# Optimization experiments

Hardware: AMD Instinct MI355X
Metric: run time of the kernel (lower is better)

The kernel has to match this reference:

```python
import jax, jax.numpy as jnp
import numpy as np
from jax import lax

# dims
B, T_MEL, N_MEL, L_TXT, D_TXT = 8, 400, 80, 128, 512
E, HID, EMB, N_SPK = 256, 256, 128, 100
H = HID // 2  # per-direction LSTM hidden


def setup_inputs() -> dict:
    key = jax.random.key(0)
    ks = jax.random.split(key, 16)
    def n(k, shape, s=0.02):
        return jax.random.normal(k, shape, jnp.float32) * s
    return {
        "x": n(ks[0], (B, N_MEL, T_MEL), 1.0),
        "input_lengths": jax.random.randint(ks[1], (B,), T_MEL // 2, T_MEL + 1).astype(jnp.int32),
        "text": n(ks[2], (B, L_TXT, D_TXT), 1.0),
        "text_lengths": jax.random.randint(ks[3], (B,), L_TXT // 2, L_TXT + 1).astype(jnp.int32),
        "Wx": n(ks[4], (E, N_MEL)), "bx": jnp.zeros((E,), jnp.float32),
        "Wq": n(ks[5], (E, D_TXT)), "bq": jnp.zeros((E,), jnp.float32),
        "Wout": n(ks[6], (E, E)), "bout": jnp.zeros((E,), jnp.float32),
        "v": jax.random.normal(ks[7], (E, 1), jnp.float32) * 0.1,
        "lstm_wih": n(ks[8], (2, 2, 4 * H, HID)),
        "lstm_whh": n(ks[9], (2, 2, 4 * H, H)),
        "lstm_bih": jnp.zeros((2, 2, 4 * H), jnp.float32),
        "lstm_bhh": jnp.zeros((2, 2, 4 * H), jnp.float32),
        "p1_w": n(ks[10], (EMB, HID)), "p1_b": jnp.zeros((EMB,), jnp.float32),
        "p2_w": n(ks[11], (N_SPK, EMB)), "p2_b": jnp.zeros((N_SPK,), jnp.float32),
    }


def _run_lstm(x, Wih, Whh, bih, bhh):
    # x: [B, L, in] -> outputs [B, L, H]; PyTorch gate order i,f,g,o
    h0 = jnp.zeros((x.shape[0], Whh.shape[1]), x.dtype)
    c0 = jnp.zeros_like(h0)
    def step(carry, xt):
        h, c = carry
        g = xt @ Wih.T + h @ Whh.T + (bih + bhh)
        i, f, gg, o = jnp.split(g, 4, axis=-1)
        c = jax.nn.sigmoid(f) * c + jax.nn.sigmoid(i) * jnp.tanh(gg)
        h = jax.nn.sigmoid(o) * jnp.tanh(c)
        return (h, c), h
    _, hs = lax.scan(step, (h0, c0), x.swapaxes(0, 1))  # scan over time
    return hs.swapaxes(0, 1)


def _reverse_by_length(x, lengths):
    # reverse the first lengths[b] steps of each sequence (pack_padded semantics)
    L = x.shape[1]
    idx = jnp.clip(lengths[:, None] - 1 - jnp.arange(L)[None, :], 0, L - 1)
    return jnp.take_along_axis(x, idx[:, :, None], axis=1)


def reference(x, input_lengths, text, text_lengths, Wx, bx, Wq, bq, Wout, bout, v,
              lstm_wih, lstm_whh, lstm_bih, lstm_bhh, p1_w, p1_b, p2_w, p2_b):
    # ---- vectorized VanillaAttention over all text tokens ----
    mels = x.swapaxes(1, 2)                       # [B, T, M]
    x1 = mels @ Wx.T + bx                         # [B, T, E]   linear_x
    q1 = text @ Wq.T + bq                         # [B, L, E]   linear_q
    # v^T @ out_linear(tanh(.)) == tanh(.) @ (Wout^T v) + v . bout
    w = Wout.T @ v[:, 0]                          # [E]
    c = bout @ v[:, 0]                            # scalar
    s = jnp.tanh(x1[:, None, :, :] + q1[:, :, None, :])   # [B, L, T, E]
    scores = jnp.einsum('blte,e->blt', s, w) + c           # [B, L, T]
    mel_mask = jnp.arange(T_MEL)[None, :] < input_lengths[:, None]   # [B, T]
    scores = jnp.where(mel_mask[:, None, :], scores, -jnp.inf)
    scores = jax.nn.softmax(scores, axis=-1)
    contexts = jnp.einsum('blt,bte->ble', scores, x1)       # [B, L, E]
    h = q1 + contexts                                       # LSTM input

    # ---- 2-layer bidirectional LSTM (packed semantics via per-length reversal) ----
    for layer in range(2):
        fwd = _run_lstm(h, lstm_wih[layer, 0], lstm_whh[layer, 0], lstm_bih[layer, 0], lstm_bhh[layer, 0])
        rev = _reverse_by_length(h, text_lengths)
        bwd = _run_lstm(rev, lstm_wih[layer, 1], lstm_whh[layer, 1], lstm_bih[layer, 1], lstm_bhh[layer, 1])
        bwd = _reverse_by_length(bwd, text_lengths)
        h = jnp.concatenate([fwd, bwd], axis=-1)            # [B, L, HID]

    # ---- masked mean pool (pad_packed zeros the padding before the sum) ----
    txt_mask = (jnp.arange(L_TXT)[None, :] < text_lengths[:, None]).astype(h.dtype)
    pooled = (h * txt_mask[:, :, None]).sum(axis=1) / text_lengths[:, None].astype(h.dtype)

    out = jnp.tanh(pooled @ p1_w.T + p1_b)
    embeddings = out / jnp.linalg.norm(out, axis=1, keepdims=True)
    logits = out @ p2_w.T + p2_b
    return logits, embeddings, scores
```

## Files before the change

### kernel.cpp

```cpp
#include <hip/hip_runtime.h>
#include <hip/hip_bf16.h>
#include <math.h>

#define B 8
#define T_MEL 400
#define N_MEL 80
#define L_TXT 128
#define D_TXT 512
#define E 256
#define HID 256
#define EMB 128
#define N_SPK 100
#define HH 128

#define OFF_W      0
#define OFF_C      256
#define OFF_WXT    272
#define OFF_WQT    (OFF_WXT + N_MEL*E)
#define OFF_WIHT   (OFF_WQT + D_TXT*E)
#define OFF_BSUM   (OFF_WIHT + 2*2*256*512)
#define OFF_X1     (OFF_BSUM + 2048)
#define OFF_Q1     (OFF_X1 + B*T_MEL*E)
#define OFF_G      OFF_X1
#define OFF_H0     (OFF_Q1 + B*L_TXT*E)
#define OFF_O1     (OFF_H0 + B*L_TXT*E)
#define OFF_HS0    OFF_H0
#define OFF_POOL   OFF_O1
#define OFF_WG     (OFF_O1 + 4096)

typedef _Float16 half2v __attribute__((ext_vector_type(2)));

__device__ __forceinline__ float fast_sigmoid(float x){ return 1.f/(1.f+__expf(-x)); }
__device__ __forceinline__ float fast_tanh(float x){ float e=__expf(2.f*x); return 1.f - 2.f/(e+1.f); }

__device__ __forceinline__ float fdot2(uint a, uint b, float c){
  half2v ha = __builtin_bit_cast(half2v, a);
  half2v hb = __builtin_bit_cast(half2v, b);
#if __has_builtin(__builtin_amdgcn_fdot2)
  return __builtin_amdgcn_fdot2(ha, hb, c, false);
#else
  float r;
  asm("v_dot2_f32_f16 %0, %1, %2, %3" : "=v"(r) : "v"(a), "v"(b), "v"(c));
  return r;
#endif
}
__device__ __forceinline__ uint packh2(float a, float b){
  union { _Float16 h[2]; uint u; } x;
  x.h[0] = (_Float16)a; x.h[1] = (_Float16)b; return x.u;
}

__global__ __launch_bounds__(256) void k_prep(const float* __restrict__ Wout, const float* __restrict__ bout,
                       const float* __restrict__ v,    const float* __restrict__ Wx,
                       const float* __restrict__ Wq,   const float* __restrict__ wih,
                       const float* __restrict__ bih,  const float* __restrict__ bhh,
                       const float* __restrict__ whh,  float* __restrict__ ws){
  int blk = blockIdx.x, tid = threadIdx.x;
  if (blk == 0){
    float acc = 0.f;
    for (int j=0;j<E;j++) acc += Wout[j*E + tid] * v[j];
    ws[OFF_W + tid] = acc;
    if (tid==0){ float c=0.f; for(int j=0;j<E;j++) c += bout[j]*v[j]; ws[OFF_C]=c; }
  } else if (blk <= N_MEL){
    int m = blk-1;
    ws[OFF_WXT + m*E + tid] = Wx[tid*N_MEL + m];
  } else if (blk <= N_MEL + D_TXT){
    int k = blk-1-N_MEL;
    ws[OFF_WQT + k*E + tid] = Wq[tid*D_TXT + k];
  } else if (blk <= N_MEL + D_TXT + 512){
    int idx = blk-1-N_MEL-D_TXT;
    int ld = idx >> 7, k2 = idx & 127;
    uint* wout = (uint*)(ws + OFF_WIHT) + (size_t)idx*512;
    for (int g = tid; g < 512; g += 256){
      float a = wih[((size_t)(ld*512+g))*256 + 2*k2];
      float b = wih[((size_t)(ld*512+g))*256 + 2*k2 + 1];
      wout[g] = packh2(a, b);
    }
  } else if (blk == 1105){
    for (int i = tid; i < 2048; i += 256)
      ws[OFF_BSUM + i] = bih[i] + bhh[i];
  } else {
    int bp = blk - 1106;
    int ld = bp >> 2, w = bp & 3;
    uint* wg = (uint*)(ws + OFF_WG) + ((size_t)ld*4 + w)*8192;
    for (int ii = 0; ii < 32; ii++){
      int i = ii*256 + tid;
      int r  = i >> 11;
      int jj = (i >> 8) & 7;
      int l  = (i >> 2) & 63;
      int k  = i & 3;
      int u  = w*32 + (l >> 1);
      int hf = l & 1;
      const float* src = whh + ((size_t)(ld*512 + r*128 + u))*HH + 64*hf + jj*8 + 2*k;
      wg[i] = packh2(src[0], src[1]);
    }
  }
}

__global__ __launch_bounds__(256) void k_xq(const float* __restrict__ x,    const float* __restrict__ bx,
                                            const float* __restrict__ text, const float* __restrict__ bq,
                                            float* __restrict__ ws){
  __shared__ float sbuf[2048];
  int blk = blockIdx.x, tid = threadIdx.x;
  if (blk < 800){
    int b = blk/100; int t0 = (blk%100)*4;
    float (*sx)[4] = (float(*)[4])sbuf;
    for (int i = tid; i < N_MEL*4; i += 256){
      int m = i>>2, ii = i&3;
      sx[m][ii] = x[(b*N_MEL+m)*T_MEL + t0 + ii];
    }
    __syncthreads();
    float bxe = bx[tid];
    float a0=bxe,a1=bxe,a2=bxe,a3=bxe;
    const float* wxt = ws + OFF_WXT;
    #pragma unroll 4
    for (int m=0;m<N_MEL;m++){
      float w = wxt[m*E + tid];
      a0 += sx[m][0]*w; a1 += sx[m][1]*w; a2 += sx[m][2]*w; a3 += sx[m][3]*w;
    }
    float* x1 = ws + OFF_X1 + (b*T_MEL + t0)*E + tid;
    x1[0]=a0; x1[E]=a1; x1[2*E]=a2; x1[3*E]=a3;
  } else {
    int bb = blk - 800;
    int b = bb/32; int l0 = (bb%32)*4;
    float (*st)[D_TXT] = (float(*)[D_TXT])sbuf;
    for (int i = tid; i < 4*D_TXT; i += 256){
      int li = i / D_TXT, k = i % D_TXT;
      st[li][k] = text[(b*L_TXT + l0 + li)*D_TXT + k];
    }
    __syncthreads();
    float bqe = bq[tid];
    float a0=bqe,a1=bqe,a2=bqe,a3=bqe;
    const float* wqt = ws + OFF_WQT;
    #pragma unroll 2
    for (int k=0;k<D_TXT;k++){
      float w = wqt[k*E + tid];
      a0 += st[0][k]*w; a1 += st[1][k]*w; a2 += st[2][k]*w; a3 += st[3][k]*w;
    }
    float* q1 = ws + OFF_Q1 + (b*L_TXT + l0)*E + tid;
    q1[0]=a0; q1[E]=a1; q1[2*E]=a2; q1[3*E]=a3;
  }
}

__global__ __launch_bounds__(256) void k_score(const int* __restrict__ mel_len,
                                               float* __restrict__ ws,
                                               float* __restrict__ d_out){
  int blk = blockIdx.x; int b = blk >> 7; int l = blk & 127;
  int tid = threadIdx.x; int lane = tid & 63; int wv = tid >> 6;
  __shared__ __align__(16) float sl[T_MEL];
  __shared__ float red[8];
  const float* x1 = ws + OFF_X1 + b*T_MEL*E;
  const float* q1 = ws + OFF_Q1 + (b*L_TXT+l)*E;
  int g = lane >> 4, i = lane & 15;
  float qv[16], wvv[16];
  {
    const float4* q4 = (const float4*)(q1 + i*16);
    const float4* w4 = (const float4*)(ws + OFF_W + i*16);
    #pragma unroll
    for (int j=0;j<4;j++){
      float4 a = q4[j]; qv[4*j]=a.x; qv[4*j+1]=a.y; qv[4*j+2]=a.z; qv[4*j+3]=a.w;
      float4 c = w4[j]; wvv[4*j]=c.x; wvv[4*j+1]=c.y; wvv[4*j+2]=c.z; wvv[4*j+3]=c.w;
    }
  }
  float cc = ws[OFF_C];
  int len = mel_len[b];
  #pragma unroll 2
  for (int iter=0; iter<25; iter++){
    int t = iter*16 + wv*4 + g;
    const float4* xr = (const float4*)(x1 + t*E + i*16);
    float s = 0.f;
    #pragma unroll
    for (int j=0;j<4;j++){
      float4 xv = xr[j];
      s += wvv[4*j+0]*fast_tanh(xv.x + qv[4*j+0]);
      s += wvv[4*j+1]*fast_tanh(xv.y + qv[4*j+1]);
      s += wvv[4*j+2]*fast_tanh(xv.z + qv[4*j+2]);
      s += wvv[4*j+3]*fast_tanh(xv.w + qv[4*j+3]);
    }
    s += __shfl_xor(s,1); s += __shfl_xor(s,2);
    s += __shfl_xor(s,4); s += __shfl_xor(s,8);
    if (i==0) sl[t] = s + cc;
  }
  __syncthreads();
  float mx = -3.0e38f;
  for (int t = tid; t < T_MEL; t += 256) if (t < len) mx = fmaxf(mx, sl[t]);
  #pragma unroll
  for (int off=32; off>=1; off>>=1) mx = fmaxf(mx, __shfl_xor(mx, off));
  if (lane==0) red[wv] = mx;
  __syncthreads();
  mx = fmaxf(fmaxf(red[0],red[1]),fmaxf(red[2],red[3]));
  float se = 0.f;
  for (int t = tid; t < T_MEL; t += 256){
    float p = (t < len) ? __expf(sl[t]-mx) : 0.f;
    sl[t] = p; se += p;
  }
  #pragma unroll
  for (int off=32; off>=1; off>>=1) se += __shfl_xor(se, off);
  if (lane==0) red[4+wv] = se;
  __syncthreads();
  float rsum = 1.f/(red[4]+red[5]+red[6]+red[7]);
  float* sc_out = d_out + 1824 + (b*L_TXT + l)*T_MEL;
  for (int t = tid; t < T_MEL; t += 256){
    float p = sl[t]*rsum;
    sl[t] = p; sc_out[t] = p;
  }
  __syncthreads();
  float a = 0.f;
  int e = tid;
  for (int t = 0; t < T_MEL; t += 4){
    float4 p4 = *(const float4*)&sl[t];
    a += p4.x*x1[(t  )*E+e] + p4.y*x1[(t+1)*E+e]
       + p4.z*x1[(t+2)*E+e] + p4.w*x1[(t+3)*E+e];
  }
  ws[OFF_H0 + (b*L_TXT+l)*E + e] = q1[e] + a;
}

__global__ __launch_bounds__(512) void k_gates(const float* __restrict__ in,
                                               const float* __restrict__ hs,
                                               const int* __restrict__ txt_len,
                                               float* __restrict__ gates, int layer,
                                               float* __restrict__ ws){
  int idx = blockIdx.x; int tt = idx & 15; int dir = (idx>>4)&1; int b = idx>>5;
  int tid = threadIdx.x;
  __shared__ __align__(16) uint sih[8][128];
  int len = txt_len[b];
  for (int i = tid; i < 8*128; i += 512){
    int r = i >> 7, k2 = i & 127;
    int t = tt*8 + r;
    int row = dir ? max(0, len-1-t) : t;
    float va, vb;
    if (layer == 0){
      const float2 p = *(const float2*)&in[((size_t)(b*L_TXT + row))*HID + 2*k2];
      va = p.x; vb = p.y;
    } else {
      int k = 2*k2; int d = k >> 7, u = k & 127;
      int sidx = (d==0) ? row : (row < len ? len-1-row : 0);
      const float* hr = hs + (((size_t)(d*8+b)*128) + u)*128 + sidx;
      va = hr[0]; vb = hr[128];
    }
    sih[r][k2] = packh2(va, vb);
  }
  __syncthreads();
  int ld = layer*2 + dir;
  int g = tid;
  float bsum = ws[OFF_BSUM + ld*512 + g];
  float acc[8];
  #pragma unroll
  for (int r=0;r<8;r++) acc[r] = bsum;
  const uint* wt2 = (const uint*)(ws + OFF_WIHT) + (size_t)ld*128*512 + g;
  for (int k4=0; k4<128; k4+=4){
    uint w0 = wt2[(k4  )*512];
    uint w1 = wt2[(k4+1)*512];
    uint w2 = wt2[(k4+2)*512];
    uint w3 = wt2[(k4+3)*512];
    #pragma unroll
    for (int r=0;r<8;r++){
      uint4 s4 = *(const uint4*)&sih[r][k4];
      acc[r] = fdot2(s4.x, w0, acc[r]);
      acc[r] = fdot2(s4.y, w1, acc[r]);
      acc[r] = fdot2(s4.z, w2, acc[r]);
      acc[r] = fdot2(s4.w, w3, acc[r]);
    }
  }
  float* go = gates + (((size_t)(dir*L_TXT + tt*8)*8) + b)*512 + g;
  #pragma unroll
  for (int r=0;r<8;r++) go[(size_t)r*8*512] = acc[r];
}

__global__ __launch_bounds__(256) void k_scan(const float* __restrict__ Gp,
                                              const float* __restrict__ whh_all,
                                              const uint* __restrict__ wg,
                                              const int* __restrict__ txt_len,
                                              float* __restrict__ hseq,
                                              float* __restrict__ pooled, int layer){
  int dir = blockIdx.x & 1; int b = blockIdx.x >> 1;
  int tid = threadIdx.x;
  int l = tid & 63, w = tid >> 6;
  int u  = tid >> 1;
  int hf = tid & 1;

  __shared__ uint wlds[16384];
  __shared__ uint h2buf[2][64];

  const float* wbase = whh_all + (size_t)(layer*2+dir)*512*HH;
  #pragma unroll
  for (int r=0;r<2;r++){
    const float* wr = wbase + (size_t)(r*128+u)*HH + 64*hf;
    #pragma unroll
    for (int jj=0;jj<8;jj++){
      uint4 vv;
      vv.x = packh2(wr[jj*8+0], wr[jj*8+1]);
      vv.y = packh2(wr[jj*8+2], wr[jj*8+3]);
      vv.z = packh2(wr[jj*8+4], wr[jj*8+5]);
      vv.w = packh2(wr[jj*8+6], wr[jj*8+7]);
      *(uint4*)(wlds + w*4096 + (r*8+jj)*256 + l*4) = vv;
    }
  }
  if (tid < 128) ((uint*)h2buf)[tid] = 0;
  int len = txt_len[b];
  bool pool = (layer == 1);

  const float* gb = Gp + ((size_t)(dir*L_TXT)*8 + b)*512 + u;
  float g0 = gb[0], g1 = gb[128], g2 = gb[256], g3 = gb[384];
  float c_reg = 0.f, psum = 0.f;
  float hm1=0.f, hm2=0.f, hm3=0.f;
  __syncthreads();

  const uint4* wp  = (const uint4*)(wlds + w*4096 + l*4);
  const uint*  wgp = wg + (((size_t)(layer*2+dir))*4 + w)*8192 + l*4;
  float* hout = hseq + (((size_t)(dir*8+b)*128) + u)*128;

  for (int s=0; s<L_TXT; s++){
    const float* gn = gb + (size_t)(s+1 < L_TXT ? s+1 : s)*4096;
    float n0 = gn[0], n1 = gn[128], n2 = gn[256], n3 = gn[384];
    const uint4* hp = (const uint4*)(h2buf[s&1] + hf*32);
    float a0 = hf ? 0.f : g0;
    float a1 = hf ? 0.f : g1;
    float a2 = hf ? 0.f : g2;
    float a3 = hf ? 0.f : g3;
    #pragma unroll
    for (int jj=0;jj<8;jj++){
      uint4 hv = hp[jj];
      uint4 w0 = wp[(jj   )*64];
      uint4 w1 = wp[( 8+jj)*64];
      uint4 w2 = *(const uint4*)(wgp + (16+jj)*256);
      uint4 w3 = *(const uint4*)(wgp + (24+jj)*256);
      a0 = fdot2(w0.x,hv.x,a0); a0 = fdot2(w0.y,hv.y,a0);
      a0 = fdot2(w0.z,hv.z,a0); a0 = fdot2(w0.w,hv.w,a0);
      a1 = fdot2(w1.x,hv.x,a1); a1 = fdot2(w1.y,hv.y,a1);
      a1 = fdot2(w1.z,hv.z,a1); a1 = fdot2(w1.w,hv.w,a1);
      a2 = fdot2(w2.x,hv.x,a2); a2 = fdot2(w2.y,hv.y,a2);
      a2 = fdot2(w2.z,hv.z,a2); a2 = fdot2(w2.w,hv.w,a2);
      a3 = fdot2(w3.x,hv.x,a3); a3 = fdot2(w3.y,hv.y,a3);
      a3 = fdot2(w3.z,hv.z,a3); a3 = fdot2(w3.w,hv.w,a3);
    }
    a0 += __shfl_xor(a0, 1);
    a1 += __shfl_xor(a1, 1);
    a2 += __shfl_xor(a2, 1);
    a3 += __shfl_xor(a3, 1);
    float i_ = fast_sigmoid(a0);
    float f_ = fast_sigmoid(a1);
    float g_ = fast_tanh   (a2);
    float o_ = fast_sigmoid(a3);
    c_reg = f_*c_reg + i_*g_;
    float h = o_*fast_tanh(c_reg);
    float hn = __shfl_xor(h, 2);
    if (hf==0 && !(u&1)) h2buf[(s+1)&1][u>>1] = packh2(h, hn);
    if (pool){
      if (s < len) psum += h;
    } else {
      if (hf==0 && (s&3)==3)
        *(float4*)&hout[s-3] = make_float4(hm3, hm2, hm1, h);
      hm3 = hm2; hm2 = hm1; hm1 = h;
    }
    g0 = n0; g1 = n1; g2 = n2; g3 = n3;
    __syncthreads();
  }
  if (pool && hf==0) pooled[((size_t)(dir*8+b))*128 + u] = psum;
}

__global__ __launch_bounds__(256) void k_final(const float* __restrict__ pooled,
                                               const int* __restrict__ txt_len,
                                               const float* __restrict__ p1w,
                                               const float* __restrict__ p1b,
                                               const float* __restrict__ p2w,
                                               const float* __restrict__ p2b,
                                               float* __restrict__ d_out){
  int b = blockIdx.x; int tid = threadIdx.x;
  __shared__ float pl[HID];
  __shared__ float ol[EMB];
  __shared__ float nrm;
  int len = txt_len[b];
  int d = tid >> 7, u = tid & 127;
  pl[tid] = pooled[((size_t)(d*8+b))*128 + u] / (float)len;
  __syncthreads();
  if (tid < EMB){
    float a = p1b[tid];
    for (int k=0;k<HID;k++) a += pl[k]*p1w[tid*HID+k];
    ol[tid] = fast_tanh(a);
  }
  __syncthreads();
  if (tid == 0){
    float q = 0.f;
    for (int k=0;k<EMB;k++) q += ol[k]*ol[k];
    nrm = rsqrtf(q);
  }
  __syncthreads();
  if (tid < EMB) d_out[800 + b*EMB + tid] = ol[tid]*nrm;
  if (tid < N_SPK){
    float a = p2b[tid];
    for (int k=0;k<EMB;k++) a += ol[k]*p2w[tid*EMB+k];
    d_out[b*N_SPK + tid] = a;
  }
}

extern "C" void kernel_launch(void* const* d_in, const int* in_sizes, int n_in,
                              void* d_out, int out_size, void* d_ws, size_t ws_size,
                              hipStream_t stream) {
  const float* x       = (const float*)d_in[0];
  const int*   mel_len = (const int*)  d_in[1];
  const float* text    = (const float*)d_in[2];
  const int*   txt_len = (const int*)  d_in[3];
  const float* Wx      = (const float*)d_in[4];
  const float* bx      = (const float*)d_in[5];
  const float* Wq      = (const float*)d_in[6];
  const float* bq      = (const float*)d_in[7];
  const float* Wout    = (const float*)d_in[8];
  const float* bout    = (const float*)d_in[9];
  const float* v       = (const float*)d_in[10];
  const float* wih     = (const float*)d_in[11];
  const float* whh     = (const float*)d_in[12];
  const float* bih     = (const float*)d_in[13];
  const float* bhh     = (const float*)d_in[14];
  const float* p1w     = (const float*)d_in[15];
  const float* p1b     = (const float*)d_in[16];
  const float* p2w     = (const float*)d_in[17];
  const float* p2b     = (const float*)d_in[18];
  float* ws  = (float*)d_ws;
  float* out = (float*)d_out;
  const uint* wg = (const uint*)(ws + OFF_WG);

  k_prep <<<1122, 256, 0, stream>>>(Wout, bout, v, Wx, Wq, wih, bih, bhh, whh, ws);
  k_xq   <<<1056, 256, 0, stream>>>(x, bx, text, bq, ws);
  k_score<<<1024, 256, 0, stream>>>(mel_len, ws, out);

  float* G = ws + OFF_G;
  k_gates<<<256, 512, 0, stream>>>(ws + OFF_H0, ws + OFF_HS0, txt_len, G, 0, ws);
  k_scan <<<16, 256, 0, stream>>>(G, whh, wg, txt_len, ws + OFF_HS0, ws + OFF_POOL, 0);
  k_gates<<<256, 512, 0, stream>>>(ws + OFF_H0, ws + OFF_HS0, txt_len, G, 1, ws);
  k_scan <<<16, 256, 0, stream>>>(G, whh, wg, txt_len, ws + OFF_HS0, ws + OFF_POOL, 1);

  k_final<<<8, 256, 0, stream>>>(ws + OFF_POOL, txt_len, p1w, p1b, p2w, p2b, out);
}
```

Before: 429.4 us.

## Tile prep transposes, keep scan gate weights in registers, retime hseq layout

```diff
diff --git a/kernel.cpp b/kernel.cpp
--- a/kernel.cpp
+++ b/kernel.cpp
@@ -54,32 +54,57 @@
                        const float* __restrict__ Wq,   const float* __restrict__ wih,
                        const float* __restrict__ bih,  const float* __restrict__ bhh,
                        const float* __restrict__ whh,  float* __restrict__ ws){
+  __shared__ __align__(16) float tile[64][81];
+  __shared__ __align__(16) uint  utile[64][129];
   int blk = blockIdx.x, tid = threadIdx.x;
   if (blk == 0){
     float acc = 0.f;
     for (int j=0;j<E;j++) acc += Wout[j*E + tid] * v[j];
     ws[OFF_W + tid] = acc;
     if (tid==0){ float c=0.f; for(int j=0;j<E;j++) c += bout[j]*v[j]; ws[OFF_C]=c; }
-  } else if (blk <= N_MEL){
-    int m = blk-1;
-    ws[OFF_WXT + m*E + tid] = Wx[tid*N_MEL + m];
-  } else if (blk <= N_MEL + D_TXT){
-    int k = blk-1-N_MEL;
-    ws[OFF_WQT + k*E + tid] = Wq[tid*D_TXT + k];
-  } else if (blk <= N_MEL + D_TXT + 512){
-    int idx = blk-1-N_MEL-D_TXT;
-    int ld = idx >> 7, k2 = idx & 127;
-    uint* wout = (uint*)(ws + OFF_WIHT) + (size_t)idx*512;
-    for (int g = tid; g < 512; g += 256){
-      float a = wih[((size_t)(ld*512+g))*256 + 2*k2];
-      float b = wih[((size_t)(ld*512+g))*256 + 2*k2 + 1];
-      wout[g] = packh2(a, b);
-    }
-  } else if (blk == 1105){
+  } else if (blk <= 4){
+    int e0 = (blk-1)*64;
+    for (int idx = tid; idx < 64*20; idx += 256){
+      int e = idx/20, c4 = idx%20;
+      float4 vv = *(const float4*)&Wx[(size_t)(e0+e)*N_MEL + 4*c4];
+      tile[e][4*c4]=vv.x; tile[e][4*c4+1]=vv.y; tile[e][4*c4+2]=vv.z; tile[e][4*c4+3]=vv.w;
+    }
+    __syncthreads();
+    for (int idx = tid; idx < N_MEL*64; idx += 256){
+      int m = idx>>6, e = idx&63;
+      ws[OFF_WXT + m*E + e0 + e] = tile[e][m];
+    }
+  } else if (blk <= 36){
+    int t = blk-5; int e0 = (t&3)*64, k0 = (t>>2)*64;
+    for (int idx = tid; idx < 64*16; idx += 256){
+      int e = idx>>4, c = idx&15;
+      float4 vv = *(const float4*)&Wq[(size_t)(e0+e)*D_TXT + k0 + 4*c];
+      tile[e][4*c]=vv.x; tile[e][4*c+1]=vv.y; tile[e][4*c+2]=vv.z; tile[e][4*c+3]=vv.w;
+    }
+    __syncthreads();
+    for (int idx = tid; idx < 64*64; idx += 256){
+      int k = idx>>6, e = idx&63;
+      ws[OFF_WQT + (k0+k)*E + e0 + e] = tile[e][k];
+    }
+  } else if (blk <= 68){
+    int t = blk-37; int ld = t>>3, g0 = (t&7)*64;
+    for (int idx = tid; idx < 64*64; idx += 256){
+      int g = idx>>6, c = idx&63;
+      float4 vv = *(const float4*)&wih[((size_t)(ld*512+g0+g))*256 + 4*c];
+      utile[g][2*c]   = packh2(vv.x, vv.y);
+      utile[g][2*c+1] = packh2(vv.z, vv.w);
+    }
+    __syncthreads();
+    uint* wout = (uint*)(ws + OFF_WIHT) + (size_t)ld*128*512;
+    for (int idx = tid; idx < 128*64; idx += 256){
+      int k2 = idx>>6, g = idx&63;
+      wout[(size_t)k2*512 + g0 + g] = utile[g][k2];
+    }
+  } else if (blk == 69){
     for (int i = tid; i < 2048; i += 256)
       ws[OFF_BSUM + i] = bih[i] + bhh[i];
   } else {
-    int bp = blk - 1106;
+    int bp = blk - 70;
     int ld = bp >> 2, w = bp & 3;
     uint* wg = (uint*)(ws + OFF_WG) + ((size_t)ld*4 + w)*8192;
     for (int ii = 0; ii < 32; ii++){
@@ -234,8 +259,8 @@
     } else {
       int k = 2*k2; int d = k >> 7, u = k & 127;
       int sidx = (d==0) ? row : (row < len ? len-1-row : 0);
-      const float* hr = hs + (((size_t)(d*8+b)*128) + u)*128 + sidx;
-      va = hr[0]; vb = hr[128];
+      const float2 p = *(const float2*)&hs[(((size_t)d*L_TXT + sidx)*8 + b)*128 + u];
+      va = p.x; vb = p.y;
     }
     sih[r][k2] = packh2(va, vb);
   }
@@ -278,7 +303,7 @@
   int u  = tid >> 1;
   int hf = tid & 1;
 
-  __shared__ uint wlds[16384];
+  __shared__ uint wlds[24576];
   __shared__ uint h2buf[2][64];
 
   const float* wbase = whh_all + (size_t)(layer*2+dir)*512*HH;
@@ -299,15 +324,25 @@
   int len = txt_len[b];
   bool pool = (layer == 1);
 
+  const uint* wgp = wg + (((size_t)(layer*2+dir))*4 + w)*8192 + l*4;
+  uint4 wg2[8], wg3[8];
+  #pragma unroll
+  for (int jj=0;jj<8;jj++){
+    wg2[jj] = *(const uint4*)(wgp + (16+jj)*256);
+    wg3[jj] = *(const uint4*)(wgp + (24+jj)*256);
+  }
+  #pragma unroll
+  for (int jj=0;jj<8;jj++){
+    asm volatile("" : "+v"(wg2[jj].x), "+v"(wg2[jj].y), "+v"(wg2[jj].z), "+v"(wg2[jj].w));
+    asm volatile("" : "+v"(wg3[jj].x), "+v"(wg3[jj].y), "+v"(wg3[jj].z), "+v"(wg3[jj].w));
+  }
+
   const float* gb = Gp + ((size_t)(dir*L_TXT)*8 + b)*512 + u;
   float g0 = gb[0], g1 = gb[128], g2 = gb[256], g3 = gb[384];
   float c_reg = 0.f, psum = 0.f;
-  float hm1=0.f, hm2=0.f, hm3=0.f;
-  __syncthreads();
-
-  const uint4* wp  = (const uint4*)(wlds + w*4096 + l*4);
-  const uint*  wgp = wg + (((size_t)(layer*2+dir))*4 + w)*8192 + l*4;
-  float* hout = hseq + (((size_t)(dir*8+b)*128) + u)*128;
+  __syncthreads();
+
+  const uint4* wp = (const uint4*)(wlds + w*4096 + l*4);
 
   for (int s=0; s<L_TXT; s++){
     const float* gn = gb + (size_t)(s+1 < L_TXT ? s+1 : s)*4096;
@@ -322,8 +357,8 @@
       uint4 hv = hp[jj];
       uint4 w0 = wp[(jj   )*64];
       uint4 w1 = wp[( 8+jj)*64];
-      uint4 w2 = *(const uint4*)(wgp + (16+jj)*256);
-      uint4 w3 = *(const uint4*)(wgp + (24+jj)*256);
+      uint4 w2 = wg2[jj];
+      uint4 w3 = wg3[jj];
       a0 = fdot2(w0.x,hv.x,a0); a0 = fdot2(w0.y,hv.y,a0);
       a0 = fdot2(w0.z,hv.z,a0); a0 = fdot2(w0.w,hv.w,a0);
       a1 = fdot2(w1.x,hv.x,a1); a1 = fdot2(w1.y,hv.y,a1);
@@ -348,9 +383,7 @@
     if (pool){
       if (s < len) psum += h;
     } else {
-      if (hf==0 && (s&3)==3)
-        *(float4*)&hout[s-3] = make_float4(hm3, hm2, hm1, h);
-      hm3 = hm2; hm2 = hm1; hm1 = h;
+      if (hf==0) hseq[(((size_t)dir*L_TXT + s)*8 + b)*128 + u] = h;
     }
     g0 = n0; g1 = n1; g2 = n2; g3 = n3;
     __syncthreads();
@@ -419,7 +452,7 @@
   float* out = (float*)d_out;
   const uint* wg = (const uint*)(ws + OFF_WG);
 
-  k_prep <<<1122, 256, 0, stream>>>(Wout, bout, v, Wx, Wq, wih, bih, bhh, whh, ws);
+  k_prep <<<86, 256, 0, stream>>>(Wout, bout, v, Wx, Wq, wih, bih, bhh, whh, ws);
   k_xq   <<<1056, 256, 0, stream>>>(x, bx, text, bq, ws);
   k_score<<<1024, 256, 0, stream>>>(mel_len, ws, out);
 
```

Result: no change. 425.8 us (-0.8%).
